# Kernel tuning notes

Measured on AMD Instinct MI355X. Metric: run time of the kernel, lower is better.

## Reference

```python
import jax, jax.numpy as jnp
import numpy as np

N_NODES = 50000
N_EDGES = 800000
HEADS = 4
OUT_CH = 32
EDGE_EMB = 4
NEG_SLOPE = 0.2


def setup_inputs() -> dict:
    key = jax.random.key(0)
    ks = jax.random.split(key, 6)
    x = jax.random.normal(ks[0], (N_NODES, 128), dtype=jnp.float32)
    edge_index = jax.random.randint(ks[1], (2, N_EDGES), 0, N_NODES, dtype=jnp.int32)
    edge_attr = jax.random.normal(ks[2], (N_EDGES, 8), dtype=jnp.float32)
    W = jax.random.normal(ks[3], (128, HEADS * OUT_CH), dtype=jnp.float32) * 0.08
    We = jax.random.normal(ks[4], (8, HEADS * EDGE_EMB), dtype=jnp.float32) * 0.3
    att = jax.random.normal(ks[5], (1, HEADS, 2 * OUT_CH + EDGE_EMB), dtype=jnp.float32) * 0.1
    bias = jnp.zeros((HEADS * OUT_CH,), dtype=jnp.float32)
    return {"x": x, "edge_index": edge_index, "edge_attr": edge_attr,
            "W": W, "We": We, "att": att, "bias": bias}


def reference(x, edge_index, edge_attr, W, We, att, bias):
    # x: [N, Din], edge_index: [2, E] (row 0 = source j, row 1 = target i)
    src = edge_index[0]
    dst = edge_index[1]
    n = x.shape[0]

    xh = (x @ W).reshape(n, HEADS, OUT_CH)                    # [N, H, O]
    eh = (edge_attr @ We).reshape(-1, HEADS, EDGE_EMB)        # [E, H, P]

    a_i = att[0, :, :OUT_CH]                                  # [H, O]
    a_j = att[0, :, OUT_CH:2 * OUT_CH]                        # [H, O]
    a_e = att[0, :, 2 * OUT_CH:]                              # [H, P]

    # per-node dot with att halves, then gather per edge (avoids [E,H,O] concat)
    s_i = jnp.einsum('nho,ho->nh', xh, a_i)                   # [N, H]
    s_j = jnp.einsum('nho,ho->nh', xh, a_j)                   # [N, H]
    s_e = jnp.einsum('ehp,hp->eh', eh, a_e)                   # [E, H]

    alpha = s_i[dst] + s_j[src] + s_e                         # [E, H]
    alpha = jax.nn.leaky_relu(alpha, NEG_SLOPE)

    # segment softmax over incoming edges of each target node
    m = jax.ops.segment_max(alpha, dst, num_segments=n)       # [N, H]
    m = jnp.where(jnp.isfinite(m), m, 0.0)
    ea = jnp.exp(alpha - m[dst])                              # [E, H]
    denom = jax.ops.segment_sum(ea, dst, num_segments=n)      # [N, H]
    alpha = ea / (denom[dst] + 1e-16)                         # [E, H]

    msg = xh[src] * alpha[:, :, None]                         # [E, H, O]
    aggr = jax.ops.segment_sum(msg, dst, num_segments=n)      # [N, H, O]
    out = aggr.reshape(n, HEADS * OUT_CH) + bias              # concat heads
    return out
```

## Files before the change

### kernel.cpp

```cpp
#include <hip/hip_runtime.h>
#include <stdint.h>
#include <math.h>

#define NEG_SLOPE 0.2f

static __device__ __forceinline__ unsigned short f2bf(float f) {
    unsigned u = __float_as_uint(f);
    unsigned r = (u + 0x7FFFu + ((u >> 16) & 1u)) >> 16;
    return (unsigned short)r;
}

__global__ __launch_bounds__(256, 3) void k_gemm_scatter(
    const float* __restrict__ x, const float* __restrict__ W,
    const float* __restrict__ att, unsigned short* __restrict__ xh16,
    float* __restrict__ s_i, float* __restrict__ s_j, int n, int GB,
    const int* __restrict__ ei, const float* __restrict__ edge_attr,
    const float* __restrict__ We, int* __restrict__ cnt, int* __restrict__ pad,
    float* __restrict__ se_edge, int E) {
    if (blockIdx.x >= GB) {
        __shared__ float ceS[32];
        int t = threadIdx.x;
        if (t < 32) {
            int k = t >> 2, h = t & 3;
            float s = 0.f;
            #pragma unroll
            for (int p = 0; p < 4; ++p)
                s += We[k * 16 + h * 4 + p] * att[h * 68 + 64 + p];
            ceS[t] = s;
        }
        __syncthreads();
        int e = (blockIdx.x - GB) * 256 + t;
        if (e < E) {
            float4 ea0 = *(const float4*)(edge_attr + (size_t)e * 8);
            float4 ea1 = *(const float4*)(edge_attr + (size_t)e * 8 + 4);
            float eav[8] = {ea0.x, ea0.y, ea0.z, ea0.w, ea1.x, ea1.y, ea1.z, ea1.w};
            float se[4];
            #pragma unroll
            for (int h = 0; h < 4; ++h) {
                float s = 0.f;
                #pragma unroll
                for (int k = 0; k < 8; ++k) s += eav[k] * ceS[k * 4 + h];
                se[h] = s;
            }
            *(float4*)(se_edge + (size_t)e * 4) = make_float4(se[0], se[1], se[2], se[3]);
            int dst = ei[E + e];
            int p = atomicAdd(&cnt[dst], 1);
            if (p < 64) pad[(size_t)dst * 64 + p] = e;
        }
        return;
    }
    __shared__ float wT[128 * 68];
    __shared__ float xS[64 * 68];
    int t = threadIdx.x;
    int c4 = t & 31;
    int rg = t >> 5;
    int r0 = blockIdx.x * 64;

    float acc[8][4];
    #pragma unroll
    for (int r = 0; r < 8; ++r)
        #pragma unroll
        for (int j = 0; j < 4; ++j) acc[r][j] = 0.f;

    for (int ch = 0; ch < 2; ++ch) {
        #pragma unroll
        for (int i = 0; i < 8; ++i) {
            int idx = t + i * 256;
            int kk = idx >> 5;
            int cq = idx & 31;
            float4 v = *(const float4*)(W + (size_t)(ch * 64 + kk) * 128 + cq * 4);
            wT[(4 * cq + 0) * 68 + kk] = v.x;
            wT[(4 * cq + 1) * 68 + kk] = v.y;
            wT[(4 * cq + 2) * 68 + kk] = v.z;
            wT[(4 * cq + 3) * 68 + kk] = v.w;
        }
        #pragma unroll
        for (int i = 0; i < 4; ++i) {
            int idx = t + i * 256;
            int r = idx >> 4;
            int q = idx & 15;
            int row = r0 + r;
            float4 v = make_float4(0.f, 0.f, 0.f, 0.f);
            if (row < n) v = *(const float4*)(x + (size_t)row * 128 + ch * 64 + q * 4);
            *(float4*)(xS + r * 68 + q * 4) = v;
        }
        __syncthreads();
        #pragma unroll 1
        for (int q = 0; q < 16; ++q) {
            float4 w0 = *(const float4*)(wT + (c4 +  0) * 68 + q * 4);
            float4 w1 = *(const float4*)(wT + (c4 + 32) * 68 + q * 4);
            float4 w2 = *(const float4*)(wT + (c4 + 64) * 68 + q * 4);
            float4 w3 = *(const float4*)(wT + (c4 + 96) * 68 + q * 4);
            #pragma unroll
            for (int r = 0; r < 8; ++r) {
                float4 xv = *(const float4*)(xS + (rg * 8 + r) * 68 + q * 4);
                acc[r][0] += xv.x * w0.x + xv.y * w0.y + xv.z * w0.z + xv.w * w0.w;
                acc[r][1] += xv.x * w1.x + xv.y * w1.y + xv.z * w1.z + xv.w * w1.w;
                acc[r][2] += xv.x * w2.x + xv.y * w2.y + xv.z * w2.z + xv.w * w2.w;
                acc[r][3] += xv.x * w3.x + xv.y * w3.y + xv.z * w3.z + xv.w * w3.w;
            }
        }
        __syncthreads();
    }

    float ai[4], aj[4];
    #pragma unroll
    for (int j = 0; j < 4; ++j) {
        ai[j] = att[j * 68 + c4];
        aj[j] = att[j * 68 + 32 + c4];
    }
    #pragma unroll 1
    for (int r = 0; r < 8; ++r) {
        int row = r0 + rg * 8 + r;
        bool ok = row < n;
        if (ok) {
            #pragma unroll
            for (int j = 0; j < 4; ++j)
                xh16[(size_t)row * 128 + c4 + 32 * j] = f2bf(acc[r][j]);
        }
        float p[8];
        #pragma unroll
        for (int j = 0; j < 4; ++j) {
            p[j] = acc[r][j] * ai[j];
            p[4 + j] = acc[r][j] * aj[j];
        }
        #pragma unroll
        for (int m = 1; m < 32; m <<= 1) {
            #pragma unroll
            for (int i = 0; i < 8; ++i) p[i] += __shfl_xor(p[i], m);
        }
        if (c4 == 0 && ok) {
            *(float4*)(s_i + (size_t)row * 4) = make_float4(p[0], p[1], p[2], p[3]);
            *(float4*)(s_j + (size_t)row * 4) = make_float4(p[4], p[5], p[6], p[7]);
        }
    }
}

__global__ __launch_bounds__(256) void k_aggr(
    const int* __restrict__ cnt, const int* __restrict__ pad,
    const float* __restrict__ se_edge, const int* __restrict__ ei,
    const float* __restrict__ s_i, const float* __restrict__ s_j,
    const unsigned* __restrict__ xh16, const float* __restrict__ bias,
    float* __restrict__ out, int n) {
    int wid = threadIdx.x >> 6;
    int l = threadIdx.x & 63;
    int node = blockIdx.x * 4 + wid;
    if (node >= n) return;
    int deg = cnt[node];
    deg = deg < 64 ? deg : 64;
    float2 b = ((const float2*)bias)[l];
    float2* op = (float2*)(out + (size_t)node * 128);

    int slot = l >> 2, h = l & 3;
    float si_h = s_i[(size_t)node * 4 + h];
    float lg[4];
    int sr[4];
    int rounds = (deg + 15) >> 4;
    #pragma unroll
    for (int r = 0; r < 4; ++r) {
        lg[r] = -INFINITY;
        sr[r] = 0;
        if (r < rounds) {
            int s = r * 16 + slot;
            if (s < deg) {
                int e = pad[(size_t)node * 64 + s];
                int src = ei[e];
                sr[r] = src;
                float sj = s_j[(size_t)src * 4 + h];
                float se = se_edge[(size_t)e * 4 + h];
                float a = si_h + sj + se;
                lg[r] = a > 0.f ? a : NEG_SLOPE * a;
            }
        }
    }
    float mx = fmaxf(fmaxf(lg[0], lg[1]), fmaxf(lg[2], lg[3]));
    #pragma unroll
    for (int m = 4; m < 64; m <<= 1) mx = fmaxf(mx, __shfl_xor(mx, m));
    float w[4];
    float sm = 0.f;
    #pragma unroll
    for (int r = 0; r < 4; ++r) {
        float ea = (r * 16 + slot < deg) ? __expf(lg[r] - mx) : 0.f;
        w[r] = ea;
        sm += ea;
    }
    #pragma unroll
    for (int m = 4; m < 64; m <<= 1) sm += __shfl_xor(sm, m);
    float rinv = 1.f / (sm + 1e-16f);
    #pragma unroll
    for (int r = 0; r < 4; ++r) w[r] *= rinv;

    int hsel = l >> 4;
    float a0 = 0.f, a1 = 0.f;
    #pragma unroll
    for (int r = 0; r < 4; ++r) {
        if (r >= rounds) break;
        int cr = deg - r * 16;
        cr = cr < 16 ? cr : 16;
        int j = 0;
        for (; j + 4 <= cr; j += 4) {
            int s0 = __shfl(sr[r], (j + 0) << 2);
            int s1 = __shfl(sr[r], (j + 1) << 2);
            int s2 = __shfl(sr[r], (j + 2) << 2);
            int s3 = __shfl(sr[r], (j + 3) << 2);
            unsigned u0 = xh16[(size_t)s0 * 64 + l];
            unsigned u1 = xh16[(size_t)s1 * 64 + l];
            unsigned u2 = xh16[(size_t)s2 * 64 + l];
            unsigned u3 = xh16[(size_t)s3 * 64 + l];
            float w0 = __shfl(w[r], (((j + 0) << 2) | hsel));
            float w1 = __shfl(w[r], (((j + 1) << 2) | hsel));
            float w2 = __shfl(w[r], (((j + 2) << 2) | hsel));
            float w3 = __shfl(w[r], (((j + 3) << 2) | hsel));
            a0 += w0 * __uint_as_float(u0 << 16);
            a1 += w0 * __uint_as_float(u0 & 0xffff0000u);
            a0 += w1 * __uint_as_float(u1 << 16);
            a1 += w1 * __uint_as_float(u1 & 0xffff0000u);
            a0 += w2 * __uint_as_float(u2 << 16);
            a1 += w2 * __uint_as_float(u2 & 0xffff0000u);
            a0 += w3 * __uint_as_float(u3 << 16);
            a1 += w3 * __uint_as_float(u3 & 0xffff0000u);
        }
        for (; j < cr; ++j) {
            int s0 = __shfl(sr[r], j << 2);
            unsigned u0 = xh16[(size_t)s0 * 64 + l];
            float w0 = __shfl(w[r], ((j << 2) | hsel));
            a0 += w0 * __uint_as_float(u0 << 16);
            a1 += w0 * __uint_as_float(u0 & 0xffff0000u);
        }
    }
    op[l] = make_float2(a0 + b.x, a1 + b.y);
}

extern "C" void kernel_launch(void* const* d_in, const int* in_sizes, int n_in,
                              void* d_out, int out_size, void* d_ws, size_t ws_size,
                              hipStream_t stream) {
    const float* x    = (const float*)d_in[0];
    const int*   ei   = (const int*)d_in[1];
    const float* eattr= (const float*)d_in[2];
    const float* W    = (const float*)d_in[3];
    const float* We   = (const float*)d_in[4];
    const float* att  = (const float*)d_in[5];
    const float* bias = (const float*)d_in[6];
    float* out = (float*)d_out;
    int n = in_sizes[0] / 128;
    int E = in_sizes[1] / 2;

    char* w = (char*)d_ws;
    auto alloc = [&](size_t bytes) {
        char* p = w;
        w += (bytes + 255) & ~(size_t)255;
        return (void*)p;
    };
    unsigned short* xh16 = (unsigned short*)alloc((size_t)n * 128 * 2);
    float* s_i           = (float*)alloc((size_t)n * 16);
    float* s_j           = (float*)alloc((size_t)n * 16);
    float* se_edge       = (float*)alloc((size_t)E * 16);
    int* cnt             = (int*)alloc((size_t)n * 4);
    int* pad             = (int*)alloc((size_t)n * 64 * 4);

    int GB = (n + 63) / 64;
    int EB = (E + 255) / 256;

    (void)hipMemsetAsync(cnt, 0, (size_t)n * 4, stream);
    k_gemm_scatter<<<GB + EB, 256, 0, stream>>>(x, W, att, xh16, s_i, s_j, n, GB,
                                                ei, eattr, We, cnt, pad, se_edge, E);
    k_aggr<<<(n + 3) / 4, 256, 0, stream>>>(cnt, pad, se_edge, ei, s_i, s_j,
                                            (const unsigned*)xh16, bias, out, n);
}
```

Before: 221.9 us.

## Shrink GEMM LDS tiles for occupancy and batch all 16 gathers per round

The GEMM path now stages W directly in natural layout, with no transpose, in 32-wide K chunks. This shrinks shared memory so the launch bound can request 6 blocks per CU instead of 3. The aggregation loop drops the degree-bounded remainder loops and always issues all 16 source gathers per round up front, raising memory-level parallelism. The cost is extra loads for padded slots in partially filled rounds. Correctness depends on padded slot indices being valid and their weights being zero.

```diff
diff --git a/kernel.cpp b/kernel.cpp
--- a/kernel.cpp
+++ b/kernel.cpp
@@ -10,7 +10,7 @@
     return (unsigned short)r;
 }
 
-__global__ __launch_bounds__(256, 3) void k_gemm_scatter(
+__global__ __launch_bounds__(256, 6) void k_gemm_scatter(
     const float* __restrict__ x, const float* __restrict__ W,
     const float* __restrict__ att, unsigned short* __restrict__ xh16,
     float* __restrict__ s_i, float* __restrict__ s_j, int n, int GB,
@@ -49,8 +49,8 @@
         }
         return;
     }
-    __shared__ float wT[128 * 68];
-    __shared__ float xS[64 * 68];
+    __shared__ float wS[32 * 128];
+    __shared__ float xS[64 * 32];
     int t = threadIdx.x;
     int c4 = t & 31;
     int rg = t >> 5;
@@ -62,42 +62,39 @@
         #pragma unroll
         for (int j = 0; j < 4; ++j) acc[r][j] = 0.f;
 
-    for (int ch = 0; ch < 2; ++ch) {
-        #pragma unroll
-        for (int i = 0; i < 8; ++i) {
+    for (int ch = 0; ch < 4; ++ch) {
+        {
+            const float4* Wv = (const float4*)(W + (size_t)ch * 32 * 128);
+            #pragma unroll
+            for (int i = 0; i < 4; ++i)
+                ((float4*)wS)[t + i * 256] = Wv[t + i * 256];
+        }
+        #pragma unroll
+        for (int i = 0; i < 2; ++i) {
             int idx = t + i * 256;
-            int kk = idx >> 5;
-            int cq = idx & 31;
-            float4 v = *(const float4*)(W + (size_t)(ch * 64 + kk) * 128 + cq * 4);
-            wT[(4 * cq + 0) * 68 + kk] = v.x;
-            wT[(4 * cq + 1) * 68 + kk] = v.y;
-            wT[(4 * cq + 2) * 68 + kk] = v.z;
-            wT[(4 * cq + 3) * 68 + kk] = v.w;
-        }
-        #pragma unroll
-        for (int i = 0; i < 4; ++i) {
-            int idx = t + i * 256;
-            int r = idx >> 4;
-            int q = idx & 15;
+            int r = idx >> 3;
+            int q = idx & 7;
             int row = r0 + r;
             float4 v = make_float4(0.f, 0.f, 0.f, 0.f);
-            if (row < n) v = *(const float4*)(x + (size_t)row * 128 + ch * 64 + q * 4);
-            *(float4*)(xS + r * 68 + q * 4) = v;
+            if (row < n) v = *(const float4*)(x + (size_t)row * 128 + ch * 32 + q * 4);
+            ((float4*)xS)[idx] = v;
         }
         __syncthreads();
         #pragma unroll 1
-        for (int q = 0; q < 16; ++q) {
-            float4 w0 = *(const float4*)(wT + (c4 +  0) * 68 + q * 4);
-            float4 w1 = *(const float4*)(wT + (c4 + 32) * 68 + q * 4);
-            float4 w2 = *(const float4*)(wT + (c4 + 64) * 68 + q * 4);
-            float4 w3 = *(const float4*)(wT + (c4 + 96) * 68 + q * 4);
+        for (int q = 0; q < 8; ++q) {
+            float wv[4][4];
+            #pragma unroll
+            for (int kk = 0; kk < 4; ++kk)
+                #pragma unroll
+                for (int j = 0; j < 4; ++j)
+                    wv[kk][j] = wS[(4 * q + kk) * 128 + 32 * j + c4];
             #pragma unroll
             for (int r = 0; r < 8; ++r) {
-                float4 xv = *(const float4*)(xS + (rg * 8 + r) * 68 + q * 4);
-                acc[r][0] += xv.x * w0.x + xv.y * w0.y + xv.z * w0.z + xv.w * w0.w;
-                acc[r][1] += xv.x * w1.x + xv.y * w1.y + xv.z * w1.z + xv.w * w1.w;
-                acc[r][2] += xv.x * w2.x + xv.y * w2.y + xv.z * w2.z + xv.w * w2.w;
-                acc[r][3] += xv.x * w3.x + xv.y * w3.y + xv.z * w3.z + xv.w * w3.w;
+                float4 xv = ((const float4*)xS)[(rg * 8 + r) * 8 + q];
+                #pragma unroll
+                for (int j = 0; j < 4; ++j)
+                    acc[r][j] += xv.x * wv[0][j] + xv.y * wv[1][j]
+                               + xv.z * wv[2][j] + xv.w * wv[3][j];
             }
         }
         __syncthreads();
@@ -195,37 +192,19 @@
     #pragma unroll
     for (int r = 0; r < 4; ++r) {
         if (r >= rounds) break;
-        int cr = deg - r * 16;
-        cr = cr < 16 ? cr : 16;
-        int j = 0;
-        for (; j + 4 <= cr; j += 4) {
-            int s0 = __shfl(sr[r], (j + 0) << 2);
-            int s1 = __shfl(sr[r], (j + 1) << 2);
-            int s2 = __shfl(sr[r], (j + 2) << 2);
-            int s3 = __shfl(sr[r], (j + 3) << 2);
-            unsigned u0 = xh16[(size_t)s0 * 64 + l];
-            unsigned u1 = xh16[(size_t)s1 * 64 + l];
-            unsigned u2 = xh16[(size_t)s2 * 64 + l];
-            unsigned u3 = xh16[(size_t)s3 * 64 + l];
-            float w0 = __shfl(w[r], (((j + 0) << 2) | hsel));
-            float w1 = __shfl(w[r], (((j + 1) << 2) | hsel));
-            float w2 = __shfl(w[r], (((j + 2) << 2) | hsel));
-            float w3 = __shfl(w[r], (((j + 3) << 2) | hsel));
-            a0 += w0 * __uint_as_float(u0 << 16);
-            a1 += w0 * __uint_as_float(u0 & 0xffff0000u);
-            a0 += w1 * __uint_as_float(u1 << 16);
-            a1 += w1 * __uint_as_float(u1 & 0xffff0000u);
-            a0 += w2 * __uint_as_float(u2 << 16);
-            a1 += w2 * __uint_as_float(u2 & 0xffff0000u);
-            a0 += w3 * __uint_as_float(u3 << 16);
-            a1 += w3 * __uint_as_float(u3 & 0xffff0000u);
-        }
-        for (; j < cr; ++j) {
-            int s0 = __shfl(sr[r], j << 2);
-            unsigned u0 = xh16[(size_t)s0 * 64 + l];
-            float w0 = __shfl(w[r], ((j << 2) | hsel));
-            a0 += w0 * __uint_as_float(u0 << 16);
-            a1 += w0 * __uint_as_float(u0 & 0xffff0000u);
+        int srcs[16];
+        float ws[16];
+        #pragma unroll
+        for (int j = 0; j < 16; ++j) srcs[j] = __shfl(sr[r], j << 2);
+        #pragma unroll
+        for (int j = 0; j < 16; ++j) ws[j] = __shfl(w[r], (j << 2) | hsel);
+        unsigned u[16];
+        #pragma unroll
+        for (int j = 0; j < 16; ++j) u[j] = xh16[(size_t)srcs[j] * 64 + l];
+        #pragma unroll
+        for (int j = 0; j < 16; ++j) {
+            a0 += ws[j] * __uint_as_float(u[j] << 16);
+            a1 += ws[j] * __uint_as_float(u[j] & 0xffff0000u);
         }
     }
     op[l] = make_float2(a0 + b.x, a1 + b.y);
```

Measured after the change: 242.7 us. +9.4%, slower.
